# Kernel tuning notes

Hardware: AMD Instinct MI355X
Metric: run time of the kernel (lower is better)

Reference implementation:

```python
import jax, jax.numpy as jnp
import numpy as np

N_NODES = 100000
N_EDGES = 1600000
D = 64
H = 128
EPS = 0.0  # learn_eps=False


def setup_inputs() -> dict:
    key = jax.random.key(0)
    k1, k2, k3, k4 = jax.random.split(key, 4)
    x = jax.random.normal(k1, (N_NODES, D), dtype=jnp.float32)
    edge_index = jax.random.randint(k2, (2, N_EDGES), 0, N_NODES, dtype=jnp.int64)
    W1 = jax.random.normal(k3, (D, H), dtype=jnp.float32) * (1.0 / np.sqrt(D))
    b1 = jnp.zeros((H,), dtype=jnp.float32)
    W2 = jax.random.normal(k4, (H, D), dtype=jnp.float32) * (1.0 / np.sqrt(H))
    b2 = jnp.zeros((D,), dtype=jnp.float32)
    return {"x": x, "edge_index": edge_index, "W1": W1, "b1": b1, "W2": W2, "b2": b2}


def reference(x, edge_index, W1, b1, W2, b2):
    src, dst = edge_index[0], edge_index[1]
    # gather neighbor features and scatter-add to destination nodes
    agg = jax.ops.segment_sum(x[src], dst, num_segments=N_NODES)  # [N, D]
    out = agg + (1.0 + EPS) * x
    # GIN MLP: Linear -> ReLU -> Linear
    h = jax.nn.relu(out @ W1 + b1)
    return h @ W2 + b2
```

## Files before the change

kernel.cpp:

```cpp
#include <hip/hip_runtime.h>

#define N_NODES 100000
#define N_EDGES 1600000
#define D 64
#define H 128
#define SCAN_BS 512
#define SCAN_NBLK ((N_NODES + SCAN_BS - 1) / SCAN_BS)

#define NB 1563
#define NCHUNK 256
#define EPC (N_EDGES / NCHUNK)
#define BCAP 2560

#define MFMA_GRID 768
#define SH_STRIDE 132
#define SH16_ST 136

typedef __attribute__((ext_vector_type(8))) short short8;
typedef __attribute__((ext_vector_type(4))) float floatx4;
typedef __attribute__((ext_vector_type(4))) unsigned short ushort4_t;
typedef __attribute__((ext_vector_type(8))) unsigned short ushort8_t;

__device__ __forceinline__ unsigned short f2bf(float f) {
    unsigned u = __builtin_bit_cast(unsigned, f);
    u += 0x7FFFu + ((u >> 16) & 1u);
    return (unsigned short)(u >> 16);
}
__device__ __forceinline__ float bf2f(unsigned short u) {
    unsigned v = ((unsigned)u) << 16;
    return __builtin_bit_cast(float, v);
}

__global__ __launch_bounds__(256) void k_pre(const float4* __restrict__ x4,
                                             ushort4_t* __restrict__ y, int n4,
                                             const int* __restrict__ dst,
                                             int* __restrict__ M2,
                                             const float* __restrict__ W1,
                                             const float* __restrict__ W2,
                                             unsigned short* __restrict__ gW1b,
                                             unsigned short* __restrict__ gW2b) {
    __shared__ int hist[NB];
    int t = threadIdx.x, blk = blockIdx.x;
    if (blk < NCHUNK) {
        int c = blk;
        for (int i = t; i < NB; i += 256) hist[i] = 0;
        __syncthreads();
        const int* dp = dst + c * EPC;
        for (int i = t; i < EPC; i += 256) atomicAdd(&hist[dp[i] >> 6], 1);
        __syncthreads();
        int* mp = M2 + c * NB;
        for (int i = t; i < NB; i += 256) mp[i] = hist[i];
    } else if (blk == NCHUNK) {
        for (int q = t; q < 8192; q += 256) {
            int j = q & 7, l = (q >> 3) & 63, f = q >> 9;
            int nt = f & 7, kt = f >> 3;
            int k = kt * 32 + ((l >> 4) << 3) + j;
            int n = nt * 16 + (l & 15);
            gW1b[q] = f2bf(W1[k * H + n]);
        }
    } else if (blk == NCHUNK + 1) {
        for (int q = t; q < 8192; q += 256) {
            int j = q & 7, l = (q >> 3) & 63, f = q >> 9;
            int nt = f & 3, kt = f >> 2;
            int k = kt * 32 + ((l >> 4) << 3) + j;
            int n = nt * 16 + (l & 15);
            gW2b[q] = f2bf(W2[k * D + n]);
        }
    } else {
        int cb = blk - NCHUNK - 2;
        int nconv = gridDim.x - NCHUNK - 2;
        for (int i = cb * 256 + t; i < n4; i += nconv * 256) {
            float4 v = x4[i];
            ushort4_t o;
            o[0] = f2bf(v.x); o[1] = f2bf(v.y); o[2] = f2bf(v.z); o[3] = f2bf(v.w);
            y[i] = o;
        }
    }
}

__global__ __launch_bounds__(256) void k_colscan(int* __restrict__ M2,
                                                 int* __restrict__ colsum) {
    int b = blockIdx.x * 256 + threadIdx.x;
    if (b >= NB) return;
    int run = 0;
    for (int c = 0; c < NCHUNK; c++) {
        int v = M2[c * NB + b];
        M2[c * NB + b] = run;
        run += v;
    }
    colsum[b] = run;
}

__global__ __launch_bounds__(256) void k_part2(const int* __restrict__ src,
                                               const int* __restrict__ dst,
                                               const int* __restrict__ M2,
                                               const int* __restrict__ colsum,
                                               int* __restrict__ ebuf,
                                               int* __restrict__ gbends) {
    __shared__ int cur[NB];
    __shared__ int sbends[NB];
    __shared__ int spart[256];
    int t = threadIdx.x, c = blockIdx.x;

    int base = t * 7;
    int v[7];
    int s = 0;
#pragma unroll
    for (int j = 0; j < 7; j++) {
        int idx = base + j;
        v[j] = (idx < NB) ? colsum[idx] : 0;
        s += v[j];
    }
    spart[t] = s;
    __syncthreads();
    for (int off = 1; off < 256; off <<= 1) {
        int u = (t >= off) ? spart[t - off] : 0;
        __syncthreads();
        spart[t] += u;
        __syncthreads();
    }
    int run = (t > 0) ? spart[t - 1] : 0;
#pragma unroll
    for (int j = 0; j < 7; j++) {
        int idx = base + j;
        run += v[j];
        if (idx < NB) sbends[idx] = run;
    }
    __syncthreads();

    const int* mp = M2 + c * NB;
    for (int i = t; i < NB; i += 256)
        cur[i] = ((i > 0) ? sbends[i - 1] : 0) + mp[i];
    if (c == 0)
        for (int i = t; i < NB; i += 256) gbends[i] = sbends[i];
    __syncthreads();

    const int* sp = src + c * EPC;
    const int* dp = dst + c * EPC;
    for (int i = t; i < EPC; i += 256) {
        int d = dp[i], srcv = sp[i];
        int p = atomicAdd(&cur[d >> 6], 1);
        ebuf[p] = srcv | ((d & 63) << 17);
    }
}

__global__ __launch_bounds__(256) void k_bagg5(const float* __restrict__ x,
                                               const unsigned short* __restrict__ x16,
                                               const int* __restrict__ ebuf,
                                               const int* __restrict__ gbends,
                                               unsigned short* __restrict__ o16) {
    __shared__ int scur[64];
    __shared__ int snd[64];
    __shared__ int slist[BCAP];
    int t = threadIdx.x, b = blockIdx.x;
    int estart = (b > 0) ? gbends[b - 1] : 0;
    int ne = gbends[b] - estart;
    const int* ep = ebuf + estart;

    int g = t >> 3;
    int l8 = t & 7;
    float aA0[8], aB0[8], aA1[8], aB1[8];
#pragma unroll
    for (int j = 0; j < 8; j++) { aA0[j] = 0.f; aB0[j] = 0.f; aA1[j] = 0.f; aB1[j] = 0.f; }

    int ntile = (ne + BCAP - 1) / BCAP;
    for (int T = 0; T < ntile; T++) {
        int toff = T * BCAP;
        int tn = ne - toff;
        if (tn > BCAP) tn = BCAP;
        __syncthreads();
        if (t < 64) scur[t] = 0;
        __syncthreads();
        for (int i = t; i < tn; i += 256) atomicAdd(&scur[ep[toff + i] >> 17], 1);
        __syncthreads();
        if (t < 64) {
            int v = scur[t], s = v;
#pragma unroll
            for (int off = 1; off < 64; off <<= 1) {
                int u = __shfl_up(s, off, 64);
                if (t >= off) s += u;
            }
            snd[t] = s;
            scur[t] = s - v;
        }
        __syncthreads();
        for (int i = t; i < tn; i += 256) {
            int v = ep[toff + i];
            int p = atomicAdd(&scur[v >> 17], 1);
            slist[p] = v & 0x1FFFF;
        }
        __syncthreads();

        {
            int dlow = g * 2;
            int s0 = (dlow > 0) ? snd[dlow - 1] : 0;
            int e1 = snd[dlow];
            int i2 = s0;
            for (; i2 + 2 <= e1; i2 += 2) {
                int sA = slist[i2], sB = slist[i2 + 1];
                ushort8_t uA = *(const ushort8_t*)&x16[(size_t)sA * D + l8 * 8];
                ushort8_t uB = *(const ushort8_t*)&x16[(size_t)sB * D + l8 * 8];
#pragma unroll
                for (int j = 0; j < 8; j++) aA0[j] += bf2f(uA[j]);
#pragma unroll
                for (int j = 0; j < 8; j++) aB0[j] += bf2f(uB[j]);
            }
            for (; i2 < e1; i2++) {
                ushort8_t uA = *(const ushort8_t*)&x16[(size_t)slist[i2] * D + l8 * 8];
#pragma unroll
                for (int j = 0; j < 8; j++) aA0[j] += bf2f(uA[j]);
            }
        }
        {
            int dlow = g * 2 + 1;
            int s0 = snd[dlow - 1];
            int e1 = snd[dlow];
            int i2 = s0;
            for (; i2 + 2 <= e1; i2 += 2) {
                int sA = slist[i2], sB = slist[i2 + 1];
                ushort8_t uA = *(const ushort8_t*)&x16[(size_t)sA * D + l8 * 8];
                ushort8_t uB = *(const ushort8_t*)&x16[(size_t)sB * D + l8 * 8];
#pragma unroll
                for (int j = 0; j < 8; j++) aA1[j] += bf2f(uA[j]);
#pragma unroll
                for (int j = 0; j < 8; j++) aB1[j] += bf2f(uB[j]);
            }
            for (; i2 < e1; i2++) {
                ushort8_t uA = *(const ushort8_t*)&x16[(size_t)slist[i2] * D + l8 * 8];
#pragma unroll
                for (int j = 0; j < 8; j++) aA1[j] += bf2f(uA[j]);
            }
        }
    }

#pragma unroll
    for (int k = 0; k < 2; k++) {
        int node = b * 64 + g * 2 + k;
        if (node < N_NODES) {
            const float* xp = x + (size_t)node * D + l8 * 8;
            float4 x0 = *(const float4*)xp;
            float4 x1 = *(const float4*)(xp + 4);
            float* pa = (k == 0) ? aA0 : aA1;
            float* pb = (k == 0) ? aB0 : aB1;
            ushort8_t o;
            o[0] = f2bf(pa[0] + pb[0] + x0.x);
            o[1] = f2bf(pa[1] + pb[1] + x0.y);
            o[2] = f2bf(pa[2] + pb[2] + x0.z);
            o[3] = f2bf(pa[3] + pb[3] + x0.w);
            o[4] = f2bf(pa[4] + pb[4] + x1.x);
            o[5] = f2bf(pa[5] + pb[5] + x1.y);
            o[6] = f2bf(pa[6] + pb[6] + x1.z);
            o[7] = f2bf(pa[7] + pb[7] + x1.w);
            *(ushort8_t*)&o16[(size_t)node * D + l8 * 8] = o;
        }
    }
}

__global__ __launch_bounds__(256) void k_mlp16(const unsigned short* __restrict__ in16,
                                               float* __restrict__ outp,
                                               const unsigned short* __restrict__ gW1b,
                                               const unsigned short* __restrict__ gW2b,
                                               const float* __restrict__ b1,
                                               const float* __restrict__ b2) {
    __shared__ unsigned short sW1b[8192];
    __shared__ unsigned short sW2b[8192];
    __shared__ unsigned short sh16[4][16 * SH16_ST];
    __shared__ float sb1[H];
    __shared__ float sb2[D];

    int t = threadIdx.x;
    for (int q = t; q < 1024; q += 256) {
        *(short8*)&sW1b[q * 8] = *(const short8*)&gW1b[q * 8];
        *(short8*)&sW2b[q * 8] = *(const short8*)&gW2b[q * 8];
    }
    if (t < H) sb1[t] = b1[t];
    if (t >= H && t < H + D) sb2[t - H] = b2[t - H];
    __syncthreads();

    int w = t >> 6, l = t & 63;
    int m = l & 15, q4 = l >> 4;
    unsigned short* shw = sh16[w];

    const int NT16 = N_NODES / 16;
    const int WAVES = MFMA_GRID * 4;
    const int ITERS = (NT16 + WAVES - 1) / WAVES;

    for (int it = 0; it < ITERS; ++it) {
        int tl = it * WAVES + blockIdx.x * 4 + w;
        bool valid = tl < NT16;
        int nbase = tl * 16;

        if (valid) {
            const unsigned short* xr = in16 + (size_t)(nbase + m) * D + q4 * 8;
            short8 A0 = *(const short8*)(xr);
            short8 A1 = *(const short8*)(xr + 32);

#pragma unroll
            for (int nt = 0; nt < 8; nt++) {
                float bv = sb1[nt * 16 + m];
                floatx4 acc = {bv, bv, bv, bv};
                short8 B0 = *(const short8*)&sW1b[(0 * 8 + nt) * 512 + l * 8];
                short8 B1 = *(const short8*)&sW1b[(1 * 8 + nt) * 512 + l * 8];
                acc = __builtin_amdgcn_mfma_f32_16x16x32_bf16(A0, B0, acc, 0, 0, 0);
                acc = __builtin_amdgcn_mfma_f32_16x16x32_bf16(A1, B1, acc, 0, 0, 0);
#pragma unroll
                for (int r = 0; r < 4; r++)
                    shw[(q4 * 4 + r) * SH16_ST + nt * 16 + m] = f2bf(fmaxf(acc[r], 0.f));
            }
        }
        __syncthreads();

        if (valid) {
            short8 Ah[4];
#pragma unroll
            for (int kt = 0; kt < 4; kt++)
                Ah[kt] = *(const short8*)&shw[m * SH16_ST + kt * 32 + q4 * 8];
#pragma unroll
            for (int nt = 0; nt < 4; nt++) {
                float bv = sb2[nt * 16 + m];
                floatx4 acc = {bv, bv, bv, bv};
#pragma unroll
                for (int kt = 0; kt < 4; kt++) {
                    short8 B = *(const short8*)&sW2b[(kt * 4 + nt) * 512 + l * 8];
                    acc = __builtin_amdgcn_mfma_f32_16x16x32_bf16(Ah[kt], B, acc, 0, 0, 0);
                }
#pragma unroll
                for (int r = 0; r < 4; r++)
                    outp[(size_t)(nbase + q4 * 4 + r) * D + nt * 16 + m] = acc[r];
            }
        }
        __syncthreads();
    }
}

__global__ __launch_bounds__(256) void k_zero(int* __restrict__ p, int n) {
    int i = blockIdx.x * 256 + threadIdx.x;
    if (i < n) p[i] = 0;
}

__global__ __launch_bounds__(256) void k_mlp_f32(float* __restrict__ io,
                                                 const float* __restrict__ W1,
                                                 const float* __restrict__ b1,
                                                 const float* __restrict__ W2,
                                                 const float* __restrict__ b2) {
    __shared__ unsigned short sW1b[8192];
    __shared__ unsigned short sW2b[8192];
    __shared__ float sh[4][16 * SH_STRIDE];
    __shared__ float sb1[H];
    __shared__ float sb2[D];

    int t = threadIdx.x;

    for (int q = t; q < 8192; q += 256) {
        int j = q & 7, l = (q >> 3) & 63, f = q >> 9;
        int nt = f & 7, kt = f >> 3;
        int k = kt * 32 + ((l >> 4) << 3) + j;
        int n = nt * 16 + (l & 15);
        sW1b[q] = f2bf(W1[k * H + n]);
    }
    for (int q = t; q < 8192; q += 256) {
        int j = q & 7, l = (q >> 3) & 63, f = q >> 9;
        int nt = f & 3, kt = f >> 2;
        int k = kt * 32 + ((l >> 4) << 3) + j;
        int n = nt * 16 + (l & 15);
        sW2b[q] = f2bf(W2[k * D + n]);
    }
    if (t < H) sb1[t] = b1[t];
    if (t >= H && t < H + D) sb2[t - H] = b2[t - H];
    __syncthreads();

    int w = t >> 6, l = t & 63;
    int m = l & 15, q4 = l >> 4;
    float* shw = sh[w];

    const int NT16 = N_NODES / 16;
    const int WAVES = 512 * 4;
    const int ITERS = (NT16 + WAVES - 1) / WAVES;

    for (int it = 0; it < ITERS; ++it) {
        int tl = it * WAVES + blockIdx.x * 4 + w;
        bool valid = tl < NT16;
        int nbase = tl * 16;

        if (valid) {
            const float* xr = io + (size_t)(nbase + m) * D + q4 * 8;
            float4 a0 = *(const float4*)(xr);
            float4 a1 = *(const float4*)(xr + 4);
            float4 c0 = *(const float4*)(xr + 32);
            float4 c1 = *(const float4*)(xr + 36);
            short8 A0, A1;
            A0[0] = f2bf(a0.x); A0[1] = f2bf(a0.y); A0[2] = f2bf(a0.z); A0[3] = f2bf(a0.w);
            A0[4] = f2bf(a1.x); A0[5] = f2bf(a1.y); A0[6] = f2bf(a1.z); A0[7] = f2bf(a1.w);
            A1[0] = f2bf(c0.x); A1[1] = f2bf(c0.y); A1[2] = f2bf(c0.z); A1[3] = f2bf(c0.w);
            A1[4] = f2bf(c1.x); A1[5] = f2bf(c1.y); A1[6] = f2bf(c1.z); A1[7] = f2bf(c1.w);

#pragma unroll
            for (int nt = 0; nt < 8; nt++) {
                float bv = sb1[nt * 16 + m];
                floatx4 acc = {bv, bv, bv, bv};
                short8 B0 = *(const short8*)&sW1b[(0 * 8 + nt) * 512 + l * 8];
                short8 B1 = *(const short8*)&sW1b[(1 * 8 + nt) * 512 + l * 8];
                acc = __builtin_amdgcn_mfma_f32_16x16x32_bf16(A0, B0, acc, 0, 0, 0);
                acc = __builtin_amdgcn_mfma_f32_16x16x32_bf16(A1, B1, acc, 0, 0, 0);
#pragma unroll
                for (int r = 0; r < 4; r++)
                    shw[(q4 * 4 + r) * SH_STRIDE + nt * 16 + m] = fmaxf(acc[r], 0.f);
            }
        }
        __syncthreads();

        if (valid) {
            short8 Ah[4];
#pragma unroll
            for (int kt = 0; kt < 4; kt++) {
                const float* hr = &shw[m * SH_STRIDE + kt * 32 + q4 * 8];
                float4 h0 = *(const float4*)(hr);
                float4 h1 = *(const float4*)(hr + 4);
                Ah[kt][0] = f2bf(h0.x); Ah[kt][1] = f2bf(h0.y);
                Ah[kt][2] = f2bf(h0.z); Ah[kt][3] = f2bf(h0.w);
                Ah[kt][4] = f2bf(h1.x); Ah[kt][5] = f2bf(h1.y);
                Ah[kt][6] = f2bf(h1.z); Ah[kt][7] = f2bf(h1.w);
            }
#pragma unroll
            for (int nt = 0; nt < 4; nt++) {
                float bv = sb2[nt * 16 + m];
                floatx4 acc = {bv, bv, bv, bv};
#pragma unroll
                for (int kt = 0; kt < 4; kt++) {
                    short8 B = *(const short8*)&sW2b[(kt * 4 + nt) * 512 + l * 8];
                    acc = __builtin_amdgcn_mfma_f32_16x16x32_bf16(Ah[kt], B, acc, 0, 0, 0);
                }
#pragma unroll
                for (int r = 0; r < 4; r++)
                    io[(size_t)(nbase + q4 * 4 + r) * D + nt * 16 + m] = acc[r];
            }
        }
        __syncthreads();
    }
}

__global__ __launch_bounds__(SCAN_BS) void k_scan1(const int* __restrict__ cnt,
                                                   int* __restrict__ ends,
                                                   int* __restrict__ bsum, int n) {
    __shared__ int s[SCAN_BS];
    int t = threadIdx.x, b = blockIdx.x;
    int id = b * SCAN_BS + t;
    s[t] = (id < n) ? cnt[id] : 0;
    __syncthreads();
    for (int off = 1; off < SCAN_BS; off <<= 1) {
        int u = (t >= off) ? s[t - off] : 0;
        __syncthreads();
        s[t] += u;
        __syncthreads();
    }
    if (id < n) ends[id] = s[t];
    if (t == SCAN_BS - 1) bsum[b] = s[t];
}

__global__ __launch_bounds__(256) void k_scan2(int* __restrict__ bsum, int nb) {
    __shared__ int s[256];
    int t = threadIdx.x;
    s[t] = (t < nb) ? bsum[t] : 0;
    __syncthreads();
    for (int off = 1; off < 256; off <<= 1) {
        int u = (t >= off) ? s[t - off] : 0;
        __syncthreads();
        s[t] += u;
        __syncthreads();
    }
    if (t < nb) bsum[t] = s[t];
}

__global__ __launch_bounds__(SCAN_BS) void k_scan3(int* __restrict__ ends,
                                                   const int* __restrict__ bsum, int n) {
    int t = threadIdx.x, b = blockIdx.x;
    int id = b * SCAN_BS + t;
    if (b > 0 && id < n) ends[id] += bsum[b - 1];
}

__global__ __launch_bounds__(256) void k_histpos(const int* __restrict__ dst,
                                                 int* __restrict__ cnt,
                                                 int* __restrict__ pos) {
    int e = blockIdx.x * 256 + threadIdx.x;
    if (e < N_EDGES) pos[e] = atomicAdd(&cnt[dst[e]], 1);
}

__global__ __launch_bounds__(256) void k_fill2(const int* __restrict__ src,
                                               const int* __restrict__ dst,
                                               const int* __restrict__ pos,
                                               const int* __restrict__ ends,
                                               int* __restrict__ csr) {
    int e = blockIdx.x * 256 + threadIdx.x;
    if (e >= N_EDGES) return;
    int d = dst[e];
    int start = (d > 0) ? ends[d - 1] : 0;
    csr[start + pos[e]] = src[e];
}

__global__ __launch_bounds__(256) void k_agg(const float* __restrict__ x,
                                             const int* __restrict__ csr,
                                             const int* __restrict__ ends,
                                             float* __restrict__ out) {
    int node = blockIdx.x * 4 + (threadIdx.x >> 6);
    if (node >= N_NODES) return;
    int f = threadIdx.x & 63;
    int start = (node > 0) ? ends[node - 1] : 0;
    int end = ends[node];
    float a0 = x[(size_t)node * D + f], a1 = 0.f, a2 = 0.f, a3 = 0.f;
    int e = start;
    for (; e + 4 <= end; e += 4) {
        int s0 = csr[e], s1 = csr[e + 1], s2 = csr[e + 2], s3 = csr[e + 3];
        a0 += x[(size_t)s0 * D + f];
        a1 += x[(size_t)s1 * D + f];
        a2 += x[(size_t)s2 * D + f];
        a3 += x[(size_t)s3 * D + f];
    }
    for (; e < end; e++) a0 += x[(size_t)csr[e] * D + f];
    out[(size_t)node * D + f] = (a0 + a1) + (a2 + a3);
}

__global__ __launch_bounds__(256) void k_init(const float4* __restrict__ x4,
                                              float4* __restrict__ agg4, int n4) {
    int i = blockIdx.x * 256 + threadIdx.x;
    if (i < n4) agg4[i] = x4[i];
}

__global__ __launch_bounds__(256) void k_scatter(const float4* __restrict__ x4,
                                                 const int* __restrict__ src,
                                                 const int* __restrict__ dst,
                                                 float* __restrict__ agg) {
    int gid = blockIdx.x * 256 + threadIdx.x;
    int e = gid >> 4;
    if (e >= N_EDGES) return;
    int c = gid & 15;
    float4 v = x4[src[e] * 16 + c];
    float* p = agg + (size_t)dst[e] * D + c * 4;
    atomicAdd(p + 0, v.x);
    atomicAdd(p + 1, v.y);
    atomicAdd(p + 2, v.z);
    atomicAdd(p + 3, v.w);
}

extern "C" void kernel_launch(void* const* d_in, const int* in_sizes, int n_in,
                              void* d_out, int out_size, void* d_ws, size_t ws_size,
                              hipStream_t stream) {
    const float* x  = (const float*)d_in[0];
    const int* eidx = (const int*)d_in[1];
    const float* W1 = (const float*)d_in[2];
    const float* b1 = (const float*)d_in[3];
    const float* W2 = (const float*)d_in[4];
    const float* b2 = (const float*)d_in[5];
    float* out      = (float*)d_out;

    const int* src = eidx;
    const int* dst = eidx + N_EDGES;

    int ge = (N_EDGES + 255) / 256;
    int n4 = N_NODES * D / 4;

    size_t need_A = (size_t)N_NODES * D * 2 * sizeof(unsigned short)
                  + (size_t)N_EDGES * sizeof(int)
                  + (size_t)16384 * sizeof(unsigned short)
                  + (size_t)(NCHUNK * NB + 2 * NB) * sizeof(int);
    size_t need_B = (size_t)(2 * N_NODES + 512 + 2 * N_EDGES) * sizeof(int);

    if (ws_size >= need_A) {
        unsigned short* x16 = (unsigned short*)d_ws;
        unsigned short* o16 = x16 + (size_t)N_NODES * D;
        int* ebuf   = (int*)(o16 + (size_t)N_NODES * D);
        unsigned short* gW1b = (unsigned short*)(ebuf + N_EDGES);
        unsigned short* gW2b = gW1b + 8192;
        int* M2     = (int*)(gW2b + 8192);
        int* colsum = M2 + NCHUNK * NB;
        int* gbends = colsum + NB;

        k_pre<<<NCHUNK + 2 + 2048, 256, 0, stream>>>((const float4*)x, (ushort4_t*)x16,
                                                     n4, dst, M2, W1, W2, gW1b, gW2b);
        k_colscan<<<(NB + 255) / 256, 256, 0, stream>>>(M2, colsum);
        k_part2<<<NCHUNK, 256, 0, stream>>>(src, dst, M2, colsum, ebuf, gbends);
        k_bagg5<<<NB, 256, 0, stream>>>(x, x16, ebuf, gbends, o16);
        k_mlp16<<<MFMA_GRID, 256, 0, stream>>>(o16, out, gW1b, gW2b, b1, b2);
    } else if (ws_size >= need_B) {
        int* cnt  = (int*)d_ws;
        int* ends = cnt + N_NODES;
        int* bsum = ends + N_NODES;
        int* pos  = bsum + 512;
        int* csr  = pos + N_EDGES;

        k_zero<<<(N_NODES + 255) / 256, 256, 0, stream>>>(cnt, N_NODES);
        k_histpos<<<ge, 256, 0, stream>>>(dst, cnt, pos);
        k_scan1<<<SCAN_NBLK, SCAN_BS, 0, stream>>>(cnt, ends, bsum, N_NODES);
        k_scan2<<<1, 256, 0, stream>>>(bsum, SCAN_NBLK);
        k_scan3<<<SCAN_NBLK, SCAN_BS, 0, stream>>>(ends, bsum, N_NODES);
        k_fill2<<<ge, 256, 0, stream>>>(src, dst, pos, ends, csr);
        k_agg<<<(N_NODES + 3) / 4, 256, 0, stream>>>(x, csr, ends, out);
        k_mlp_f32<<<512, 256, 0, stream>>>(out, W1, b1, W2, b2);
    } else {
        k_init<<<(n4 + 255) / 256, 256, 0, stream>>>((const float4*)x, (float4*)out, n4);
        long long total = (long long)N_EDGES * 16;
        k_scatter<<<(int)((total + 255) / 256), 256, 0, stream>>>(
            (const float4*)x, src, dst, out);
        k_mlp_f32<<<512, 256, 0, stream>>>(out, W1, b1, W2, b2);
    }
}
```

Baseline: 173.7 us.

## Fuse MLP into bucketed aggregation kernel, dropping bf16 intermediate buffer

The aggregation kernel now stages each block's 64 aggregated rows in shared memory as bf16 and runs the two-layer MFMA MLP on them directly. This removes the separate MLP launch and the global write and re-read of the 100000x64 bf16 intermediate. Weights are read from global/L2 on every MFMA instead of being staged in LDS, and the shared buffer is reused between the edge list and the hidden activations. Extra LDS and registers per block may lower occupancy of the gather phase.

```diff
diff --git a/kernel.cpp b/kernel.cpp
--- a/kernel.cpp
+++ b/kernel.cpp
@@ -12,9 +12,9 @@
 #define EPC (N_EDGES / NCHUNK)
 #define BCAP 2560
 
-#define MFMA_GRID 768
 #define SH_STRIDE 132
 #define SH16_ST 136
+#define SAGG_ST 72
 
 typedef __attribute__((ext_vector_type(8))) short short8;
 typedef __attribute__((ext_vector_type(4))) float floatx4;
@@ -144,14 +144,22 @@
     }
 }
 
-__global__ __launch_bounds__(256) void k_bagg5(const float* __restrict__ x,
+__global__ __launch_bounds__(256) void k_bagg6(const float* __restrict__ x,
                                                const unsigned short* __restrict__ x16,
                                                const int* __restrict__ ebuf,
                                                const int* __restrict__ gbends,
-                                               unsigned short* __restrict__ o16) {
+                                               const unsigned short* __restrict__ gW1b,
+                                               const unsigned short* __restrict__ gW2b,
+                                               const float* __restrict__ b1,
+                                               const float* __restrict__ b2,
+                                               float* __restrict__ outp) {
+    __shared__ __align__(16) char smem0[16 * SH16_ST * 4 * 2];
+    __shared__ __align__(16) unsigned short sagg[64][SAGG_ST];
     __shared__ int scur[64];
     __shared__ int snd[64];
-    __shared__ int slist[BCAP];
+    int* slist = (int*)smem0;
+    unsigned short* sh16 = (unsigned short*)smem0;
+
     int t = threadIdx.x, b = blockIdx.x;
     int estart = (b > 0) ? gbends[b - 1] : 0;
     int ne = gbends[b] - estart;
@@ -233,16 +241,18 @@
         }
     }
 
+    __syncthreads();
 #pragma unroll
     for (int k = 0; k < 2; k++) {
-        int node = b * 64 + g * 2 + k;
+        int nl = g * 2 + k;
+        int node = b * 64 + nl;
+        ushort8_t o;
         if (node < N_NODES) {
             const float* xp = x + (size_t)node * D + l8 * 8;
             float4 x0 = *(const float4*)xp;
             float4 x1 = *(const float4*)(xp + 4);
             float* pa = (k == 0) ? aA0 : aA1;
             float* pb = (k == 0) ? aB0 : aB1;
-            ushort8_t o;
             o[0] = f2bf(pa[0] + pb[0] + x0.x);
             o[1] = f2bf(pa[1] + pb[1] + x0.y);
             o[2] = f2bf(pa[2] + pb[2] + x0.z);
@@ -251,85 +261,55 @@
             o[5] = f2bf(pa[5] + pb[5] + x1.y);
             o[6] = f2bf(pa[6] + pb[6] + x1.z);
             o[7] = f2bf(pa[7] + pb[7] + x1.w);
-            *(ushort8_t*)&o16[(size_t)node * D + l8 * 8] = o;
-        }
-    }
-}
-
-__global__ __launch_bounds__(256) void k_mlp16(const unsigned short* __restrict__ in16,
-                                               float* __restrict__ outp,
-                                               const unsigned short* __restrict__ gW1b,
-                                               const unsigned short* __restrict__ gW2b,
-                                               const float* __restrict__ b1,
-                                               const float* __restrict__ b2) {
-    __shared__ unsigned short sW1b[8192];
-    __shared__ unsigned short sW2b[8192];
-    __shared__ unsigned short sh16[4][16 * SH16_ST];
-    __shared__ float sb1[H];
-    __shared__ float sb2[D];
-
-    int t = threadIdx.x;
-    for (int q = t; q < 1024; q += 256) {
-        *(short8*)&sW1b[q * 8] = *(const short8*)&gW1b[q * 8];
-        *(short8*)&sW2b[q * 8] = *(const short8*)&gW2b[q * 8];
-    }
-    if (t < H) sb1[t] = b1[t];
-    if (t >= H && t < H + D) sb2[t - H] = b2[t - H];
+        } else {
+            o[0] = 0; o[1] = 0; o[2] = 0; o[3] = 0;
+            o[4] = 0; o[5] = 0; o[6] = 0; o[7] = 0;
+        }
+        *(ushort8_t*)&sagg[nl][l8 * 8] = o;
+    }
     __syncthreads();
 
     int w = t >> 6, l = t & 63;
     int m = l & 15, q4 = l >> 4;
-    unsigned short* shw = sh16[w];
-
-    const int NT16 = N_NODES / 16;
-    const int WAVES = MFMA_GRID * 4;
-    const int ITERS = (NT16 + WAVES - 1) / WAVES;
-
-    for (int it = 0; it < ITERS; ++it) {
-        int tl = it * WAVES + blockIdx.x * 4 + w;
-        bool valid = tl < NT16;
-        int nbase = tl * 16;
-
-        if (valid) {
-            const unsigned short* xr = in16 + (size_t)(nbase + m) * D + q4 * 8;
-            short8 A0 = *(const short8*)(xr);
-            short8 A1 = *(const short8*)(xr + 32);
-
-#pragma unroll
-            for (int nt = 0; nt < 8; nt++) {
-                float bv = sb1[nt * 16 + m];
-                floatx4 acc = {bv, bv, bv, bv};
-                short8 B0 = *(const short8*)&sW1b[(0 * 8 + nt) * 512 + l * 8];
-                short8 B1 = *(const short8*)&sW1b[(1 * 8 + nt) * 512 + l * 8];
-                acc = __builtin_amdgcn_mfma_f32_16x16x32_bf16(A0, B0, acc, 0, 0, 0);
-                acc = __builtin_amdgcn_mfma_f32_16x16x32_bf16(A1, B1, acc, 0, 0, 0);
-#pragma unroll
-                for (int r = 0; r < 4; r++)
-                    shw[(q4 * 4 + r) * SH16_ST + nt * 16 + m] = f2bf(fmaxf(acc[r], 0.f));
-            }
-        }
-        __syncthreads();
-
-        if (valid) {
-            short8 Ah[4];
-#pragma unroll
-            for (int kt = 0; kt < 4; kt++)
-                Ah[kt] = *(const short8*)&shw[m * SH16_ST + kt * 32 + q4 * 8];
-#pragma unroll
-            for (int nt = 0; nt < 4; nt++) {
-                float bv = sb2[nt * 16 + m];
-                floatx4 acc = {bv, bv, bv, bv};
-#pragma unroll
-                for (int kt = 0; kt < 4; kt++) {
-                    short8 B = *(const short8*)&sW2b[(kt * 4 + nt) * 512 + l * 8];
-                    acc = __builtin_amdgcn_mfma_f32_16x16x32_bf16(Ah[kt], B, acc, 0, 0, 0);
-                }
-#pragma unroll
-                for (int r = 0; r < 4; r++)
-                    outp[(size_t)(nbase + q4 * 4 + r) * D + nt * 16 + m] = acc[r];
-            }
-        }
-        __syncthreads();
+    unsigned short* shw = sh16 + w * (16 * SH16_ST);
+    int nbase = b * 64 + w * 16;
+
+    short8 A0 = *(const short8*)&sagg[w * 16 + m][q4 * 8];
+    short8 A1 = *(const short8*)&sagg[w * 16 + m][32 + q4 * 8];
+
+#pragma unroll
+    for (int nt = 0; nt < 8; nt++) {
+        float bv = b1[nt * 16 + m];
+        floatx4 acc = {bv, bv, bv, bv};
+        short8 B0 = *(const short8*)&gW1b[(0 * 8 + nt) * 512 + l * 8];
+        short8 B1 = *(const short8*)&gW1b[(1 * 8 + nt) * 512 + l * 8];
+        acc = __builtin_amdgcn_mfma_f32_16x16x32_bf16(A0, B0, acc, 0, 0, 0);
+        acc = __builtin_amdgcn_mfma_f32_16x16x32_bf16(A1, B1, acc, 0, 0, 0);
+#pragma unroll
+        for (int r = 0; r < 4; r++)
+            shw[(q4 * 4 + r) * SH16_ST + nt * 16 + m] = f2bf(fmaxf(acc[r], 0.f));
+    }
+    __syncthreads();
+
+    short8 Ah[4];
+#pragma unroll
+    for (int kt = 0; kt < 4; kt++)
+        Ah[kt] = *(const short8*)&shw[m * SH16_ST + kt * 32 + q4 * 8];
+#pragma unroll
+    for (int nt = 0; nt < 4; nt++) {
+        float bv = b2[nt * 16 + m];
+        floatx4 acc = {bv, bv, bv, bv};
+#pragma unroll
+        for (int kt = 0; kt < 4; kt++) {
+            short8 B = *(const short8*)&gW2b[(kt * 4 + nt) * 512 + l * 8];
+            acc = __builtin_amdgcn_mfma_f32_16x16x32_bf16(Ah[kt], B, acc, 0, 0, 0);
+        }
+#pragma unroll
+        for (int r = 0; r < 4; r++) {
+            int row = nbase + q4 * 4 + r;
+            if (row < N_NODES)
+                outp[(size_t)row * D + nt * 16 + m] = acc[r];
+        }
     }
 }
 
@@ -558,7 +538,7 @@
     int ge = (N_EDGES + 255) / 256;
     int n4 = N_NODES * D / 4;
 
-    size_t need_A = (size_t)N_NODES * D * 2 * sizeof(unsigned short)
+    size_t need_A = (size_t)N_NODES * D * sizeof(unsigned short)
                   + (size_t)N_EDGES * sizeof(int)
                   + (size_t)16384 * sizeof(unsigned short)
                   + (size_t)(NCHUNK * NB + 2 * NB) * sizeof(int);
@@ -566,8 +546,7 @@
 
     if (ws_size >= need_A) {
         unsigned short* x16 = (unsigned short*)d_ws;
-        unsigned short* o16 = x16 + (size_t)N_NODES * D;
-        int* ebuf   = (int*)(o16 + (size_t)N_NODES * D);
+        int* ebuf   = (int*)(x16 + (size_t)N_NODES * D);
         unsigned short* gW1b = (unsigned short*)(ebuf + N_EDGES);
         unsigned short* gW2b = gW1b + 8192;
         int* M2     = (int*)(gW2b + 8192);
@@ -578,8 +557,7 @@
                                                      n4, dst, M2, W1, W2, gW1b, gW2b);
         k_colscan<<<(NB + 255) / 256, 256, 0, stream>>>(M2, colsum);
         k_part2<<<NCHUNK, 256, 0, stream>>>(src, dst, M2, colsum, ebuf, gbends);
-        k_bagg5<<<NB, 256, 0, stream>>>(x, x16, ebuf, gbends, o16);
-        k_mlp16<<<MFMA_GRID, 256, 0, stream>>>(o16, out, gW1b, gW2b, b1, b2);
+        k_bagg6<<<NB, 256, 0, stream>>>(x, x16, ebuf, gbends, gW1b, gW2b, b1, b2, out);
     } else if (ws_size >= need_B) {
         int* cnt  = (int*)d_ws;
         int* ends = cnt + N_NODES;
```

Result: slower. 184.8 us (+6.3%).
